# Performance work log

Measured on AMD Instinct MI355X. Metric: run time of the kernel, lower is better.

The kernel has to match this reference:

```python
import jax, jax.numpy as jnp
import numpy as np

B, P, U = 512, 24, 24
IN_T, IN_I, IN_O = 768, 2048, 512
INI = 512            # ini_hidden_dim for all three input linears
H = 1000             # BiLSTM hidden; embed_d = 2*H
E = 2 * H            # embed_d = 2000
INIA = 512           # agg init_linear out dim
HA = 1000            # agg BiLSTM hidden


def _bilstm1(x, W, b):
    """Single-step bidirectional LSTM from zero initial state.
    x: [..., D], W: [2, 4H, D] (fwd/bwd stacked), b: [2, 4H] (b_ih+b_hh).
    With h0=c0=0: gates = x@W_ih^T + b; c = sigmoid(i)*tanh(g); h = sigmoid(o)*tanh(c).
    Returns [..., 2H] (fwd then bwd, matching torch bidirectional concat)."""
    g = jnp.einsum('...d,khd->...kh', x, W) + b          # [..., 2, 4H]
    i, f, gg, o = jnp.split(g, 4, axis=-1)
    c = jax.nn.sigmoid(i) * jnp.tanh(gg)
    h = jax.nn.sigmoid(o) * jnp.tanh(c)                  # [..., 2, H]
    return h.reshape(h.shape[:-2] + (2 * h.shape[-1],))


def _lin(x, W, b):
    return x @ W.T + b


def setup_inputs() -> dict:
    key = jax.random.key(0)
    ks = iter(jax.random.split(key, 48))
    s = 0.05
    def w(*shape):
        return jax.random.normal(next(ks), shape, jnp.float32) * s
    def dat(*shape):
        return jax.random.normal(next(ks), shape, jnp.float32)
    inp = {
        'c_text': dat(B, IN_T), 'c_image': dat(B, IN_I),
        'p_text': dat(B, P, IN_T), 'p_image': dat(B, P, IN_I),
        'u_text': dat(B, U, IN_T), 'u_other': dat(B, U, IN_O),
        # shared per-type input linears
        'W_lt': w(INI, IN_T), 'b_lt': w(INI),
        'W_li': w(INI, IN_I), 'b_li': w(INI),
        'W_lo': w(INI, IN_O), 'b_lo': w(INI),
        # per-type BiLSTMs (fwd/bwd stacked on axis 0)
        'lstm_t_W': w(2, 4 * H, INI), 'lstm_t_b': w(2, 4 * H),
        'lstm_i_W': w(2, 4 * H, INI), 'lstm_i_b': w(2, 4 * H),
        'lstm_o_W': w(2, 4 * H, INI), 'lstm_o_b': w(2, 4 * H),
        # SameType_Agg stacks (user and post)
        'ua_lin_W': w(INIA, E), 'ua_lin_b': w(INIA),
        'ua_lstm_W': w(2, 4 * HA, INIA), 'ua_lstm_b': w(2, 4 * HA),
        'ua_out_W': w(E, 2 * HA), 'ua_out_b': w(E),
        'pa_lin_W': w(INIA, E), 'pa_lin_b': w(INIA),
        'pa_lstm_W': w(2, 4 * HA, INIA), 'pa_lstm_b': w(2, 4 * HA),
        'pa_out_W': w(E, 2 * HA), 'pa_out_b': w(E),
        # attention vector for post-type center nodes
        'p_att': w(2 * E, 1),
    }
    return inp


def reference(c_text, c_image, p_text, p_image, u_text, u_other,
              W_lt, b_lt, W_li, b_li, W_lo, b_lo,
              lstm_t_W, lstm_t_b, lstm_i_W, lstm_i_b, lstm_o_W, lstm_o_b,
              ua_lin_W, ua_lin_b, ua_lstm_W, ua_lstm_b, ua_out_W, ua_out_b,
              pa_lin_W, pa_lin_b, pa_lstm_W, pa_lstm_b, pa_out_W, pa_out_b,
              p_att):
    def post_birnn(text, image):
        # cat along seq dim of two len-1 outputs then mean over seq == average
        ht = _bilstm1(_lin(text, W_lt, b_lt), lstm_t_W, lstm_t_b)
        hi = _bilstm1(_lin(image, W_li, b_li), lstm_i_W, lstm_i_b)
        return 0.5 * (ht + hi)                            # [..., E]

    def user_birnn(text, other):
        ht = _bilstm1(_lin(text, W_lt, b_lt), lstm_t_W, lstm_t_b)
        ho = _bilstm1(_lin(other, W_lo, b_lo), lstm_o_W, lstm_o_b)
        return 0.5 * (ht + ho)

    def same_type_agg(ce, lW, lb, sW, sb, oW, ob):
        h = _bilstm1(_lin(ce, lW, lb), sW, sb)            # [B, N, 2*HA]
        out = _lin(h, oW, ob)                             # [B, N, E]
        return out.mean(axis=1)                           # mean over neighbors

    c = post_birnn(c_text, c_image)                       # [B, E] (center = post)
    u_agg = same_type_agg(user_birnn(u_text, u_other),
                          ua_lin_W, ua_lin_b, ua_lstm_W, ua_lstm_b, ua_out_W, ua_out_b)
    p_agg = same_type_agg(post_birnn(p_text, p_image),
                          pa_lin_W, pa_lin_b, pa_lstm_W, pa_lstm_b, pa_out_W, pa_out_b)

    pairs = jnp.stack([jnp.concatenate([c, c], -1),
                       jnp.concatenate([c, u_agg], -1),
                       jnp.concatenate([c, p_agg], -1)], axis=1)   # [B, 3, 2E]
    att = jax.nn.leaky_relu(pairs @ p_att, 0.01)          # [B, 3, 1]
    wts = jax.nn.softmax(att, axis=1)[..., 0]             # [B, 3]
    emb3 = jnp.stack([c, u_agg, p_agg], axis=1)           # [B, 3, E]
    return jnp.einsum('bk,bke->be', wts, emb3)            # [B, E]
```

## Files before the change

### kernel.cpp

```cpp
#include <hip/hip_runtime.h>
#include <hip/hip_bf16.h>


typedef __hip_bfloat16 bf16;
typedef __attribute__((ext_vector_type(8))) short short8;
typedef __attribute__((ext_vector_type(4))) float f32x4;

__device__ __forceinline__ float bf2f(bf16 x){ return __bfloat162float(x); }
__device__ __forceinline__ bf16  f2bf(float x){ return __float2bfloat16(x); }

__device__ __forceinline__ void gld16(const bf16* g, bf16* l){
  __builtin_amdgcn_global_load_lds(
      (const __attribute__((address_space(1))) void*)g,
      (__attribute__((address_space(3))) void*)l, 16, 0, 0);
}

__device__ __forceinline__ void barrier_raw(){ asm volatile("s_barrier" ::: "memory"); }
__device__ __forceinline__ void wait_vm0(){ asm volatile("s_waitcnt vmcnt(0)" ::: "memory"); }
__device__ __forceinline__ void wait_vm3(){ asm volatile("s_waitcnt vmcnt(3)" ::: "memory"); }
__device__ __forceinline__ void wait_vm4(){ asm volatile("s_waitcnt vmcnt(4)" ::: "memory"); }

__device__ __forceinline__ float sigm(float x){ return 1.0f/(1.0f + __expf(-x)); }
__device__ __forceinline__ float tanhfast(float x){
  x = fminf(fmaxf(x, -15.f), 15.f);
  float e = __expf(2.f*x);
  return (e-1.f)/(e+1.f);
}

struct CvtPtrs { const float* p[25]; };
__constant__ long CVT_CUM[26] = {0, 98304, 98432, 360576, 360704, 426240,
  426368, 1450368, 1452368, 2476368, 2478368, 3502368, 3504368, 3760368,
  3760496, 4784496, 4786496, 5786496, 5786996, 6042996, 6043124, 7067124,
  7069124, 8069124, 8069624, 8070624};

__global__ __launch_bounds__(256) void cvt_all(CvtPtrs P, bf16* __restrict__ arena)
{
  long g = (long)blockIdx.x * 256 + threadIdx.x;
  if (g >= 8070624l) return;
  int lo = 0, hi = 24;
  while (lo < hi) { int mid = (lo + hi + 1) >> 1; if (g >= CVT_CUM[mid]) lo = mid; else hi = mid - 1; }
  long rel = (g - CVT_CUM[lo]) * 4;
  float4 v = *(const float4*)(P.p[lo] + rel);
  union { bf16 h[4]; uint2 u; } t;
  t.h[0]=f2bf(v.x); t.h[1]=f2bf(v.y); t.h[2]=f2bf(v.z); t.h[3]=f2bf(v.w);
  *(uint2*)(arena + CVT_CUM[lo]*4 + rel) = t.u;
}

__global__ __launch_bounds__(256) void gemm_linA32(
    const float* __restrict__ A, const float* __restrict__ A2, int splitx,
    const bf16* __restrict__ Bt, const bf16* __restrict__ bias,
    bf16* __restrict__ C, int M, int N, int K, int lda, int ldb, int ldc)
{
  __shared__ bf16 sm[2][(128+128)*32];
  const int tid  = threadIdx.x;
  const int wave = tid >> 6, lane = tid & 63;
  const int wr = (wave >> 1) * 64, wc = (wave & 1) * 64;
  const int ln = lane & 15, lq = lane >> 4;
  const long m0 = (long)blockIdx.x * 128;
  const int  n0 = blockIdx.y * 128;

  const float* Abase; long mrow;
  if ((int)blockIdx.x < splitx) { Abase = A;  mrow = m0; }
  else { Abase = A2; mrow = (long)((int)blockIdx.x - splitx) * 128; }

  const int arow = tid >> 1, ahalf = (tid & 1) * 16;
  const float* pA = Abase + (mrow + arow) * (long)lda + ahalf;
  const int sAoff = arow * 32 + ahalf;
  const int ch = (tid & 3) * 8;
  int colA = n0 + (tid >> 2);       colA = (colA < N) ? colA : (N - 1);
  int colB = n0 + (tid >> 2) + 64;  colB = (colB < N) ? colB : (N - 1);
  const bf16* pB0 = Bt + (long)colA * ldb + ch;
  const bf16* pB1 = Bt + (long)colB * ldb + ch;
  const int sB0 = 128*32 + tid * 8, sB1 = 128*32 + (tid + 256) * 8;

  auto cvtA = [&](bf16* dst, float4 v0, float4 v1, float4 v2, float4 v3){
    union { bf16 h[16]; short8 q[2]; } u;
    u.h[0]=f2bf(v0.x); u.h[1]=f2bf(v0.y); u.h[2]=f2bf(v0.z); u.h[3]=f2bf(v0.w);
    u.h[4]=f2bf(v1.x); u.h[5]=f2bf(v1.y); u.h[6]=f2bf(v1.z); u.h[7]=f2bf(v1.w);
    u.h[8]=f2bf(v2.x); u.h[9]=f2bf(v2.y); u.h[10]=f2bf(v2.z); u.h[11]=f2bf(v2.w);
    u.h[12]=f2bf(v3.x); u.h[13]=f2bf(v3.y); u.h[14]=f2bf(v3.z); u.h[15]=f2bf(v3.w);
    *(short8*)(dst)     = u.q[0];
    *(short8*)(dst + 8) = u.q[1];
  };

  const int ksteps = K >> 5;
  {
    float4 v0 = *(const float4*)(pA);
    float4 v1 = *(const float4*)(pA + 4);
    float4 v2 = *(const float4*)(pA + 8);
    float4 v3 = *(const float4*)(pA + 12);
    cvtA(sm[0] + sAoff, v0, v1, v2, v3);
    gld16(pB0, sm[0] + sB0);
    gld16(pB1, sm[0] + sB1);
    pA += 32; pB0 += 32; pB1 += 32;
  }
  __syncthreads();

  f32x4 acc[4][4] = {};
  for (int ks = 0; ks < ksteps; ++ks) {
    const bf16* S = sm[ks & 1];
    bf16* Sn = sm[(ks + 1) & 1];
    const bool stage = (ks + 1 < ksteps);
    float4 v0, v1, v2, v3;
    if (stage) {
      v0 = *(const float4*)(pA);
      v1 = *(const float4*)(pA + 4);
      v2 = *(const float4*)(pA + 8);
      v3 = *(const float4*)(pA + 12);
      gld16(pB0, Sn + sB0);
      gld16(pB1, Sn + sB1);
      pA += 32; pB0 += 32; pB1 += 32;
    }
    const bf16* As = S; const bf16* Bs = S + 128*32;
    short8 af[4], bv[4];
#pragma unroll
    for (int i = 0; i < 4; ++i)
      af[i] = *(const short8*)(As + (wr + i*16 + ln) * 32 + lq * 8);
#pragma unroll
    for (int j = 0; j < 4; ++j)
      bv[j] = *(const short8*)(Bs + (wc + j*16 + ln) * 32 + lq * 8);
#pragma unroll
    for (int i = 0; i < 4; ++i)
#pragma unroll
      for (int j = 0; j < 4; ++j)
        acc[i][j] = __builtin_amdgcn_mfma_f32_16x16x32_bf16(af[i], bv[j], acc[i][j], 0, 0, 0);
    if (stage) cvtA(Sn + sAoff, v0, v1, v2, v3);
    __syncthreads();
  }
#pragma unroll
  for (int j = 0; j < 4; ++j) {
    int n = n0 + wc + j * 16 + ln;
    if (n < N) {
      float bvv = bf2f(bias[n]);
#pragma unroll
      for (int i = 0; i < 4; ++i)
#pragma unroll
        for (int r = 0; r < 4; ++r) {
          long m = m0 + wr + i * 16 + lq * 4 + r;
          C[m * ldc + n] = f2bf(acc[i][j][r] + bvv);
        }
    } else if (n < ldc) {
#pragma unroll
      for (int i = 0; i < 4; ++i)
#pragma unroll
        for (int r = 0; r < 4; ++r) {
          long m = m0 + wr + i * 16 + lq * 4 + r;
          C[m * ldc + n] = f2bf(0.f);
        }
    }
  }
}

__global__ __launch_bounds__(256) void gemm_lin(
    const bf16* __restrict__ A, const bf16* __restrict__ Bt,
    const bf16* __restrict__ bias, bf16* __restrict__ C,
    int M, int N, int K, int lda, int ldb, int ldc)
{
  __shared__ bf16 sm[2][(128+128)*32];
  const int tid  = threadIdx.x;
  const int wave = tid >> 6, lane = tid & 63;
  const int wr = (wave >> 1) * 64, wc = (wave & 1) * 64;
  const int ln = lane & 15, lq = lane >> 4;
  const long m0 = (long)blockIdx.x * 128;
  const int  n0 = blockIdx.y * 128;

  const int ch = (tid & 3) * 8;
  const bf16* pA0 = A + (m0 + (tid >> 2)) * (long)lda + ch;
  const bf16* pA1 = A + (m0 + (tid >> 2) + 64) * (long)lda + ch;
  int colA = n0 + (tid >> 2);       colA = (colA < N) ? colA : (N - 1);
  int colB = n0 + (tid >> 2) + 64;  colB = (colB < N) ? colB : (N - 1);
  const bf16* pB0 = Bt + (long)colA * ldb + ch;
  const bf16* pB1 = Bt + (long)colB * ldb + ch;
  const int sA0 = tid * 8, sA1 = (tid + 256) * 8;
  const int sB0 = 128*32 + tid * 8, sB1 = 128*32 + (tid + 256) * 8;

  const int ksteps = (K + 31) >> 5;
  {
    gld16(pA0, sm[0] + sA0); gld16(pA1, sm[0] + sA1);
    gld16(pB0, sm[0] + sB0); gld16(pB1, sm[0] + sB1);
    pA0 += 32; pA1 += 32; pB0 += 32; pB1 += 32;
  }
  __syncthreads();

  f32x4 acc[4][4] = {};
  for (int ks = 0; ks < ksteps; ++ks) {
    const bf16* S = sm[ks & 1];
    bf16* Sn = sm[(ks + 1) & 1];
    if (ks + 1 < ksteps) {
      gld16(pA0, Sn + sA0); gld16(pA1, Sn + sA1);
      gld16(pB0, Sn + sB0); gld16(pB1, Sn + sB1);
      pA0 += 32; pA1 += 32; pB0 += 32; pB1 += 32;
    }
    const bf16* As = S; const bf16* Bs = S + 128*32;
    short8 af[4], bv[4];
#pragma unroll
    for (int i = 0; i < 4; ++i)
      af[i] = *(const short8*)(As + (wr + i*16 + ln) * 32 + lq * 8);
#pragma unroll
    for (int j = 0; j < 4; ++j)
      bv[j] = *(const short8*)(Bs + (wc + j*16 + ln) * 32 + lq * 8);
#pragma unroll
    for (int i = 0; i < 4; ++i)
#pragma unroll
      for (int j = 0; j < 4; ++j)
        acc[i][j] = __builtin_amdgcn_mfma_f32_16x16x32_bf16(af[i], bv[j], acc[i][j], 0, 0, 0);
    __syncthreads();
  }
#pragma unroll
  for (int j = 0; j < 4; ++j) {
    int n = n0 + wc + j * 16 + ln;
    if (n < N) {
      float bvv = bf2f(bias[n]);
#pragma unroll
      for (int i = 0; i < 4; ++i)
#pragma unroll
        for (int r = 0; r < 4; ++r) {
          long m = m0 + wr + i * 16 + lq * 4 + r;
          C[m * ldc + n] = f2bf(acc[i][j][r] + bvv);
        }
    } else if (n < ldc) {
#pragma unroll
      for (int i = 0; i < 4; ++i)
#pragma unroll
        for (int r = 0; r < 4; ++r) {
          long m = m0 + wr + i * 16 + lq * 4 + r;
          C[m * ldc + n] = f2bf(0.f);
        }
    }
  }
}

__global__ __launch_bounds__(256) void gemm_out_f32(
    const bf16* __restrict__ A0, const bf16* __restrict__ A1,
    const bf16* __restrict__ B0, const bf16* __restrict__ B1,
    const bf16* __restrict__ b0, const bf16* __restrict__ b1,
    float* __restrict__ C0, float* __restrict__ C1)
{
  __shared__ bf16 sm[2][(128+128)*32];
  const int tid  = threadIdx.x;
  const int wave = tid >> 6, lane = tid & 63;
  const int wr = (wave >> 1) * 64, wc = (wave & 1) * 64;
  const int ln = lane & 15, lq = lane >> 4;
  const int seg = blockIdx.x >> 2;
  const long m0 = (long)(blockIdx.x & 3) * 128;
  const int  n0 = blockIdx.y * 128;
  const int N = 2000, lda = 2016, ldb = 2000, ldc = 2000;

  const bf16* A    = seg ? A1 : A0;
  const bf16* Bt   = seg ? B1 : B0;
  const bf16* bias = seg ? b1 : b0;
  float*      C    = seg ? C1 : C0;

  const int ch = (tid & 3) * 8;
  const bf16* pA0 = A + (m0 + (tid >> 2)) * (long)lda + ch;
  const bf16* pA1 = A + (m0 + (tid >> 2) + 64) * (long)lda + ch;
  int colA = n0 + (tid >> 2);       colA = (colA < N) ? colA : (N - 1);
  int colB = n0 + (tid >> 2) + 64;  colB = (colB < N) ? colB : (N - 1);
  const bf16* pB0 = Bt + (long)colA * ldb + ch;
  const bf16* pB1 = Bt + (long)colB * ldb + ch;
  const int sA0 = tid * 8, sA1 = (tid + 256) * 8;
  const int sB0 = 128*32 + tid * 8, sB1 = 128*32 + (tid + 256) * 8;

  {
    gld16(pA0, sm[0] + sA0); gld16(pA1, sm[0] + sA1);
    gld16(pB0, sm[0] + sB0); gld16(pB1, sm[0] + sB1);
    pA0 += 32; pA1 += 32; pB0 += 32; pB1 += 32;
  }
  __syncthreads();

  f32x4 acc[4][4] = {};
  for (int ks = 0; ks < 63; ++ks) {
    const bf16* S = sm[ks & 1];
    bf16* Sn = sm[(ks + 1) & 1];
    if (ks + 1 < 63) {
      gld16(pA0, Sn + sA0); gld16(pA1, Sn + sA1);
      gld16(pB0, Sn + sB0); gld16(pB1, Sn + sB1);
      pA0 += 32; pA1 += 32; pB0 += 32; pB1 += 32;
    }
    const bf16* As = S; const bf16* Bs = S + 128*32;
    short8 af[4], bv[4];
#pragma unroll
    for (int i = 0; i < 4; ++i)
      af[i] = *(const short8*)(As + (wr + i*16 + ln) * 32 + lq * 8);
#pragma unroll
    for (int j = 0; j < 4; ++j)
      bv[j] = *(const short8*)(Bs + (wc + j*16 + ln) * 32 + lq * 8);
#pragma unroll
    for (int i = 0; i < 4; ++i)
#pragma unroll
      for (int j = 0; j < 4; ++j)
        acc[i][j] = __builtin_amdgcn_mfma_f32_16x16x32_bf16(af[i], bv[j], acc[i][j], 0, 0, 0);
    __syncthreads();
  }
#pragma unroll
  for (int j = 0; j < 4; ++j) {
    int n = n0 + wc + j * 16 + ln;
    if (n < N) {
      float bvv = bf2f(bias[n]);
#pragma unroll
      for (int i = 0; i < 4; ++i)
#pragma unroll
        for (int r = 0; r < 4; ++r) {
          long m = m0 + wr + i * 16 + lq * 4 + r;
          C[m * ldc + n] = acc[i][j][r] + bvv;
        }
    }
  }
}

__global__ __launch_bounds__(256) void gemm_lstm(
    const bf16* __restrict__ A, const bf16* __restrict__ W,
    const bf16* __restrict__ bvec, const bf16* __restrict__ other,
    bf16* __restrict__ Hout, int ldo, int ldc, int combine)
{
  __shared__ bf16 sm[2][(128+96)*32];
  const int tid  = threadIdx.x;
  const int wave = tid >> 6, lane = tid & 63;
  const int wr = (wave >> 1) * 64, wc = (wave & 1) * 48;
  const int ln = lane & 15, lq = lane >> 4;
  const long m0 = (long)blockIdx.x * 128;
  const int dir = blockIdx.y >> 5, jb = blockIdx.y & 31;

  const int ch = (tid & 3) * 8;
  const bf16* pA0 = A + (m0 + (tid >> 2)) * 512 + ch;
  const bf16* pA1 = A + (m0 + (tid >> 2) + 64) * 512 + ch;
  auto brow = [&](int t) -> long {
    int tc = t >> 2;
    int grp = tc / 48, wi = tc % 48, cf = wi >> 4;
    int jj = jb * 32 + grp * 16 + (wi & 15);
    jj = (jj < 1000) ? jj : 999;
    return (long)(dir * 4000 + cf * 1000 + (cf ? 1000 : 0) + jj);
  };
  const bf16* pB0 = W + brow(tid) * 512 + ch;
  const bf16* pB1 = W + brow(tid + 256) * 512 + ch;
  const int sA0 = tid * 8, sA1 = (tid + 256) * 8;
  const int sB0 = 128*32 + tid * 8, sB1 = 128*32 + (tid + 256) * 8;
  const bool doB1 = (tid < 128);

  {
    gld16(pA0, sm[0] + sA0); gld16(pA1, sm[0] + sA1);
    gld16(pB0, sm[0] + sB0);
    if (doB1) gld16(pB1, sm[0] + sB1);
    pA0 += 32; pA1 += 32; pB0 += 32; pB1 += 32;
  }

  f32x4 acc[4][3] = {};
  for (int ks = 0; ks < 16; ++ks) {
    const bf16* S = sm[ks & 1];
    bf16* Sn = sm[(ks + 1) & 1];
    const bool stage = (ks + 1 < 16);
    if (stage) {
      gld16(pA0, Sn + sA0); gld16(pA1, Sn + sA1);
      gld16(pB0, Sn + sB0);
      if (doB1) gld16(pB1, Sn + sB1);
      pA0 += 32; pA1 += 32; pB0 += 32; pB1 += 32;
    }
    if (!stage)      wait_vm0();
    else if (doB1)   wait_vm4();
    else             wait_vm3();
    barrier_raw();
    const bf16* As = S; const bf16* Bs = S + 128*32;
    short8 af[4], bv[3];
#pragma unroll
    for (int i = 0; i < 4; ++i)
      af[i] = *(const short8*)(As + (wr + i*16 + ln) * 32 + lq * 8);
#pragma unroll
    for (int j = 0; j < 3; ++j)
      bv[j] = *(const short8*)(Bs + (wc + j*16 + ln) * 32 + lq * 8);
#pragma unroll
    for (int i = 0; i < 4; ++i)
#pragma unroll
      for (int j = 0; j < 3; ++j)
        acc[i][j] = __builtin_amdgcn_mfma_f32_16x16x32_bf16(af[i], bv[j], acc[i][j], 0, 0, 0);
    barrier_raw();
  }
  const int jj  = jb * 32 + (wave & 1) * 16 + ln;
  const int jc  = (jj < 1000) ? jj : 999;
  const float bI = bf2f(bvec[dir * 4000 + jc]);
  const float bG = bf2f(bvec[dir * 4000 + 2000 + jc]);
  const float bO = bf2f(bvec[dir * 4000 + 3000 + jc]);
  const int col = dir * 1000 + jj;
  const bool sv = (jj < 1000);
  const bool sz = (!sv) && (dir == 1) && (col < ldc);
  if (!sv && !sz) return;
#pragma unroll
  for (int i = 0; i < 4; ++i)
#pragma unroll
    for (int r = 0; r < 4; ++r) {
      long m = m0 + wr + i * 16 + lq * 4 + r;
      float h = 0.f;
      if (sv) {
        float gi = acc[i][0][r] + bI;
        float gg = acc[i][1][r] + bG;
        float go = acc[i][2][r] + bO;
        float cc = sigm(gi) * tanhfast(gg);
        h = sigm(go) * tanhfast(cc);
        if (combine) h = 0.5f * (h + bf2f(other[m * ldo + col]));
      }
      Hout[m * ldc + col] = f2bf(h);
    }
}

__global__ __launch_bounds__(256) void meanh(const bf16* __restrict__ X, bf16* __restrict__ Y)
{
  long idx = (long)blockIdx.x * 256 + threadIdx.x;
  if (idx >= 512l * 2016) return;
  long b = idx / 2016, e = idx % 2016;
  const bf16* p = X + b * 24 * 2016 + e;
  float s = 0.f;
#pragma unroll
  for (int n = 0; n < 24; ++n) s += bf2f(p[(long)n * 2016]);
  Y[idx] = f2bf(s * (1.f / 24.f));
}

__global__ __launch_bounds__(256) void attn_mix(
    const bf16* __restrict__ Cm, const float* __restrict__ U,
    const float* __restrict__ P, const float* __restrict__ att,
    float* __restrict__ out, int ldcm)
{
  const int b = blockIdx.x, tid = threadIdx.x;
  __shared__ float red[4][4];
  __shared__ float wsh[3];
  float s0 = 0, s1 = 0, s2 = 0, s3 = 0;
  const long baseC = (long)b * ldcm;
  const long base  = (long)b * 2000;
  for (int e = tid; e < 2000; e += 256) {
    float cv = bf2f(Cm[baseC + e]);
    float al = att[e];
    float ah = att[2000 + e];
    s0 += cv * al; s1 += cv * ah;
    s2 += U[base + e] * ah; s3 += P[base + e] * ah;
  }
#pragma unroll
  for (int o = 32; o; o >>= 1) {
    s0 += __shfl_down(s0, o); s1 += __shfl_down(s1, o);
    s2 += __shfl_down(s2, o); s3 += __shfl_down(s3, o);
  }
  if ((tid & 63) == 0) {
    int w = tid >> 6;
    red[w][0] = s0; red[w][1] = s1; red[w][2] = s2; red[w][3] = s3;
  }
  __syncthreads();
  if (tid == 0) {
    float a0 = 0, a1 = 0, a2 = 0, a3 = 0;
    for (int w = 0; w < 4; ++w) { a0 += red[w][0]; a1 += red[w][1]; a2 += red[w][2]; a3 += red[w][3]; }
    float t0 = a0 + a1, t1 = a0 + a2, t2 = a0 + a3;
    t0 = t0 > 0 ? t0 : 0.01f * t0;
    t1 = t1 > 0 ? t1 : 0.01f * t1;
    t2 = t2 > 0 ? t2 : 0.01f * t2;
    float mx = fmaxf(t0, fmaxf(t1, t2));
    float e0 = __expf(t0 - mx), e1 = __expf(t1 - mx), e2 = __expf(t2 - mx);
    float inv = 1.f / (e0 + e1 + e2);
    wsh[0] = e0 * inv; wsh[1] = e1 * inv; wsh[2] = e2 * inv;
  }
  __syncthreads();
  float w0 = wsh[0], w1 = wsh[1], w2 = wsh[2];
  for (int e = tid; e < 2000; e += 256)
    out[base + e] = w0 * bf2f(Cm[baseC + e]) + w1 * U[base + e] + w2 * P[base + e];
}

extern "C" void kernel_launch(void* const* d_in, const int* in_sizes, int n_in,
                              void* d_out, int out_size, void* d_ws, size_t ws_size,
                              hipStream_t stream)
{
  const float* c_text  = (const float*)d_in[0];
  const float* c_image = (const float*)d_in[1];
  const float* p_text  = (const float*)d_in[2];
  const float* p_image = (const float*)d_in[3];
  const float* u_text  = (const float*)d_in[4];
  const float* u_other = (const float*)d_in[5];
  const float* p_att   = (const float*)d_in[30];
  float* out = (float*)d_out;

  char* ws = (char*)d_ws;
  size_t off = 0;
  auto alloc = [&](size_t bytes) -> char* {
    char* p = ws + off; off += (bytes + 255) & ~(size_t)255; return p;
  };
  bf16* ARENA = (bf16*)alloc(32282496ull * 2);
  bf16* BIG1  = (bf16*)alloc(12800ull * 2016 * 2);
  bf16* BIG2  = (bf16*)alloc(12800ull * 2016 * 2);
  bf16* X1    = (bf16*)alloc(12800ull * 512 * 2);
  bf16* X2    = (bf16*)alloc(12800ull * 512 * 2);
  bf16* Yu    = (bf16*)alloc(512ull * 2016 * 2);
  bf16* Yp    = (bf16*)alloc(512ull * 2016 * 2);
  float* UA   = (float*)alloc(512ull * 2000 * 4);
  float* PA   = (float*)alloc(512ull * 2000 * 4);
  (void)ws_size; (void)in_sizes; (void)n_in; (void)out_size;

  const bf16* aW_lt = ARENA + 0;        const bf16* ab_lt = ARENA + 393216;
  const bf16* aW_li = ARENA + 393728;   const bf16* ab_li = ARENA + 1442304;
  const bf16* aW_lo = ARENA + 1442816;  const bf16* ab_lo = ARENA + 1704960;
  const bf16* alt_W = ARENA + 1705472;  const bf16* alt_b = ARENA + 5801472;
  const bf16* ali_W = ARENA + 5809472;  const bf16* ali_b = ARENA + 9905472;
  const bf16* alo_W = ARENA + 9913472;  const bf16* alo_b = ARENA + 14009472;
  const bf16* aua_lin_W  = ARENA + 14017472; const bf16* aua_lin_b  = ARENA + 15041472;
  const bf16* aua_lstm_W = ARENA + 15041984; const bf16* aua_lstm_b = ARENA + 19137984;
  const bf16* aua_out_W  = ARENA + 19145984; const bf16* aua_out_b  = ARENA + 23145984;
  const bf16* apa_lin_W  = ARENA + 23147984; const bf16* apa_lin_b  = ARENA + 24171984;
  const bf16* apa_lstm_W = ARENA + 24172496; const bf16* apa_lstm_b = ARENA + 28268496;
  const bf16* apa_out_W  = ARENA + 28276496; const bf16* apa_out_b  = ARENA + 32276496;

  CvtPtrs cp;
  for (int i = 0; i < 25; ++i) cp.p[i] = (const float*)d_in[6 + i];
  cvt_all<<<dim3(31527), dim3(256), 0, stream>>>(cp, ARENA);

  dim3 blk(256);
  const int NOSPLIT = 1 << 30;

  gemm_linA32<<<dim3(96,4), blk, 0, stream>>>(u_text,  u_text,  NOSPLIT, aW_lt, ab_lt, X1, 12288, 512, 768, 768, 768, 512);
  gemm_linA32<<<dim3(96,4), blk, 0, stream>>>(u_other, u_other, NOSPLIT, aW_lo, ab_lo, X2, 12288, 512, 512, 512, 512, 512);
  gemm_lstm<<<dim3(96,64), blk, 0, stream>>>(X1, alt_W, alt_b, nullptr, BIG1, 2016, 2016, 0);
  gemm_lstm<<<dim3(96,64), blk, 0, stream>>>(X2, alo_W, alo_b, BIG1,    BIG2, 2016, 2016, 1);
  gemm_lin<<<dim3(96,4), blk, 0, stream>>>(BIG2, aua_lin_W, aua_lin_b, X1, 12288, 512, 2000, 2016, 2000, 512);
  gemm_lstm<<<dim3(96,64), blk, 0, stream>>>(X1, aua_lstm_W, aua_lstm_b, nullptr, BIG1, 2016, 2016, 0);
  meanh<<<dim3(4032), blk, 0, stream>>>(BIG1, Yu);

  gemm_linA32<<<dim3(100,4), blk, 0, stream>>>(p_text,  c_text,  96, aW_lt, ab_lt, X1, 12800, 512, 768,  768,  768,  512);
  gemm_linA32<<<dim3(100,4), blk, 0, stream>>>(p_image, c_image, 96, aW_li, ab_li, X2, 12800, 512, 2048, 2048, 2048, 512);
  gemm_lstm<<<dim3(100,64), blk, 0, stream>>>(X1, alt_W, alt_b, nullptr, BIG1, 2016, 2016, 0);
  gemm_lstm<<<dim3(100,64), blk, 0, stream>>>(X2, ali_W, ali_b, BIG1,    BIG2, 2016, 2016, 1);
  gemm_lin<<<dim3(96,4), blk, 0, stream>>>(BIG2, apa_lin_W, apa_lin_b, X1, 12288, 512, 2000, 2016, 2000, 512);
  gemm_lstm<<<dim3(96,64), blk, 0, stream>>>(X1, apa_lstm_W, apa_lstm_b, nullptr, BIG1, 2016, 2016, 0);
  meanh<<<dim3(4032), blk, 0, stream>>>(BIG1, Yp);

  gemm_out_f32<<<dim3(8,16), blk, 0, stream>>>(Yu, Yp, aua_out_W, apa_out_W,
                                               aua_out_b, apa_out_b, UA, PA);
  attn_mix<<<dim3(512), blk, 0, stream>>>(BIG2 + 12288l * 2016, UA, PA, p_att, out, 2016);
}
```

Measured before the change: 1.490 ms.

## Widen LSTM gate GEMM tile to 64 hidden units and swizzle LDS chunks

The fused LSTM gate GEMM now computes 64 hidden units per block (192 weight rows) instead of 32, halving the grid along the hidden dimension and doubling reuse of each staged activation tile. It also XOR-swizzles the 16-byte k-chunks in LDS on both write and read, to reduce bank conflicts on the fragment loads. The cost is more accumulator registers (4x6 tiles), more LDS per block and fewer blocks, which may lower occupancy.

```diff
diff --git a/kernel.cpp b/kernel.cpp
--- a/kernel.cpp
+++ b/kernel.cpp
@@ -17,8 +17,7 @@
 
 __device__ __forceinline__ void barrier_raw(){ asm volatile("s_barrier" ::: "memory"); }
 __device__ __forceinline__ void wait_vm0(){ asm volatile("s_waitcnt vmcnt(0)" ::: "memory"); }
-__device__ __forceinline__ void wait_vm3(){ asm volatile("s_waitcnt vmcnt(3)" ::: "memory"); }
-__device__ __forceinline__ void wait_vm4(){ asm volatile("s_waitcnt vmcnt(4)" ::: "memory"); }
+__device__ __forceinline__ void wait_vm5(){ asm volatile("s_waitcnt vmcnt(5)" ::: "memory"); }
 
 __device__ __forceinline__ float sigm(float x){ return 1.0f/(1.0f + __expf(-x)); }
 __device__ __forceinline__ float tanhfast(float x){
@@ -313,92 +312,96 @@
     const bf16* __restrict__ bvec, const bf16* __restrict__ other,
     bf16* __restrict__ Hout, int ldo, int ldc, int combine)
 {
-  __shared__ bf16 sm[2][(128+96)*32];
+  __shared__ bf16 sm[2][(128+192)*32];
   const int tid  = threadIdx.x;
   const int wave = tid >> 6, lane = tid & 63;
-  const int wr = (wave >> 1) * 64, wc = (wave & 1) * 48;
+  const int wr = (wave >> 1) * 64, wc = (wave & 1) * 96;
   const int ln = lane & 15, lq = lane >> 4;
   const long m0 = (long)blockIdx.x * 128;
-  const int dir = blockIdx.y >> 5, jb = blockIdx.y & 31;
-
-  const int ch = (tid & 3) * 8;
+  const int dir = blockIdx.y >> 4, jb = blockIdx.y & 15;
+
+  const int ch = (((tid & 3) ^ ((tid >> 3) & 3))) * 8;
   const bf16* pA0 = A + (m0 + (tid >> 2)) * 512 + ch;
   const bf16* pA1 = A + (m0 + (tid >> 2) + 64) * 512 + ch;
   auto brow = [&](int t) -> long {
     int tc = t >> 2;
-    int grp = tc / 48, wi = tc % 48, cf = wi >> 4;
-    int jj = jb * 32 + grp * 16 + (wi & 15);
+    int g48 = tc / 48, wi = tc % 48;
+    int cf = wi >> 4;
+    int jj = jb * 64 + g48 * 16 + (wi & 15);
     jj = (jj < 1000) ? jj : 999;
-    return (long)(dir * 4000 + cf * 1000 + (cf ? 1000 : 0) + jj);
+    return (long)(dir * 4000 + (cf ? (cf + 1) * 1000 : 0) + jj);
   };
   const bf16* pB0 = W + brow(tid) * 512 + ch;
   const bf16* pB1 = W + brow(tid + 256) * 512 + ch;
+  const bf16* pB2 = W + brow(tid + 512) * 512 + ch;
   const int sA0 = tid * 8, sA1 = (tid + 256) * 8;
-  const int sB0 = 128*32 + tid * 8, sB1 = 128*32 + (tid + 256) * 8;
-  const bool doB1 = (tid < 128);
+  const int sB0 = 128*32 + tid * 8;
+  const int sB1 = 128*32 + (tid + 256) * 8;
+  const int sB2 = 128*32 + (tid + 512) * 8;
+  const int swz = (lq ^ ((ln >> 1) & 3)) * 8;
 
   {
     gld16(pA0, sm[0] + sA0); gld16(pA1, sm[0] + sA1);
-    gld16(pB0, sm[0] + sB0);
-    if (doB1) gld16(pB1, sm[0] + sB1);
-    pA0 += 32; pA1 += 32; pB0 += 32; pB1 += 32;
-  }
-
-  f32x4 acc[4][3] = {};
+    gld16(pB0, sm[0] + sB0); gld16(pB1, sm[0] + sB1); gld16(pB2, sm[0] + sB2);
+    pA0 += 32; pA1 += 32; pB0 += 32; pB1 += 32; pB2 += 32;
+  }
+
+  f32x4 acc[4][6] = {};
   for (int ks = 0; ks < 16; ++ks) {
     const bf16* S = sm[ks & 1];
     bf16* Sn = sm[(ks + 1) & 1];
     const bool stage = (ks + 1 < 16);
     if (stage) {
       gld16(pA0, Sn + sA0); gld16(pA1, Sn + sA1);
-      gld16(pB0, Sn + sB0);
-      if (doB1) gld16(pB1, Sn + sB1);
-      pA0 += 32; pA1 += 32; pB0 += 32; pB1 += 32;
-    }
-    if (!stage)      wait_vm0();
-    else if (doB1)   wait_vm4();
-    else             wait_vm3();
+      gld16(pB0, Sn + sB0); gld16(pB1, Sn + sB1); gld16(pB2, Sn + sB2);
+      pA0 += 32; pA1 += 32; pB0 += 32; pB1 += 32; pB2 += 32;
+    }
+    if (stage) wait_vm5(); else wait_vm0();
     barrier_raw();
     const bf16* As = S; const bf16* Bs = S + 128*32;
-    short8 af[4], bv[3];
-#pragma unroll
-    for (int i = 0; i < 4; ++i)
-      af[i] = *(const short8*)(As + (wr + i*16 + ln) * 32 + lq * 8);
-#pragma unroll
-    for (int j = 0; j < 3; ++j)
-      bv[j] = *(const short8*)(Bs + (wc + j*16 + ln) * 32 + lq * 8);
-#pragma unroll
-    for (int i = 0; i < 4; ++i)
-#pragma unroll
-      for (int j = 0; j < 3; ++j)
+    short8 af[4], bv[6];
+#pragma unroll
+    for (int i = 0; i < 4; ++i)
+      af[i] = *(const short8*)(As + (wr + i*16 + ln) * 32 + swz);
+#pragma unroll
+    for (int j = 0; j < 6; ++j)
+      bv[j] = *(const short8*)(Bs + (wc + j*16 + ln) * 32 + swz);
+#pragma unroll
+    for (int i = 0; i < 4; ++i)
+#pragma unroll
+      for (int j = 0; j < 6; ++j)
         acc[i][j] = __builtin_amdgcn_mfma_f32_16x16x32_bf16(af[i], bv[j], acc[i][j], 0, 0, 0);
     barrier_raw();
   }
-  const int jj  = jb * 32 + (wave & 1) * 16 + ln;
-  const int jc  = (jj < 1000) ? jj : 999;
-  const float bI = bf2f(bvec[dir * 4000 + jc]);
-  const float bG = bf2f(bvec[dir * 4000 + 2000 + jc]);
-  const float bO = bf2f(bvec[dir * 4000 + 3000 + jc]);
-  const int col = dir * 1000 + jj;
-  const bool sv = (jj < 1000);
-  const bool sz = (!sv) && (dir == 1) && (col < ldc);
-  if (!sv && !sz) return;
-#pragma unroll
-  for (int i = 0; i < 4; ++i)
-#pragma unroll
-    for (int r = 0; r < 4; ++r) {
-      long m = m0 + wr + i * 16 + lq * 4 + r;
-      float h = 0.f;
-      if (sv) {
-        float gi = acc[i][0][r] + bI;
-        float gg = acc[i][1][r] + bG;
-        float go = acc[i][2][r] + bO;
-        float cc = sigm(gi) * tanhfast(gg);
-        h = sigm(go) * tanhfast(cc);
-        if (combine) h = 0.5f * (h + bf2f(other[m * ldo + col]));
+  const int hbase = jb * 64 + (wave & 1) * 32;
+#pragma unroll
+  for (int jg = 0; jg < 2; ++jg) {
+    const int jj = hbase + jg * 16 + ln;
+    const int jc = (jj < 1000) ? jj : 999;
+    const float bI = bf2f(bvec[dir * 4000 + jc]);
+    const float bG = bf2f(bvec[dir * 4000 + 2000 + jc]);
+    const float bO = bf2f(bvec[dir * 4000 + 3000 + jc]);
+    const int col = dir * 1000 + jj;
+    const bool sv = (jj < 1000);
+    const bool sz = (!sv) && (dir == 1) && (col < ldc);
+    if (!sv && !sz) continue;
+#pragma unroll
+    for (int i = 0; i < 4; ++i)
+#pragma unroll
+      for (int r = 0; r < 4; ++r) {
+        long m = m0 + wr + i * 16 + lq * 4 + r;
+        float h = 0.f;
+        if (sv) {
+          float gi = acc[i][jg*3+0][r] + bI;
+          float gg = acc[i][jg*3+1][r] + bG;
+          float go = acc[i][jg*3+2][r] + bO;
+          float cc = sigm(gi) * tanhfast(gg);
+          h = sigm(go) * tanhfast(cc);
+          if (combine) h = 0.5f * (h + bf2f(other[m * ldo + col]));
+        }
+        Hout[m * ldc + col] = f2bf(h);
       }
-      Hout[m * ldc + col] = f2bf(h);
-    }
+  }
 }
 
 __global__ __launch_bounds__(256) void meanh(const bf16* __restrict__ X, bf16* __restrict__ Y)
@@ -510,18 +513,18 @@
 
   gemm_linA32<<<dim3(96,4), blk, 0, stream>>>(u_text,  u_text,  NOSPLIT, aW_lt, ab_lt, X1, 12288, 512, 768, 768, 768, 512);
   gemm_linA32<<<dim3(96,4), blk, 0, stream>>>(u_other, u_other, NOSPLIT, aW_lo, ab_lo, X2, 12288, 512, 512, 512, 512, 512);
-  gemm_lstm<<<dim3(96,64), blk, 0, stream>>>(X1, alt_W, alt_b, nullptr, BIG1, 2016, 2016, 0);
-  gemm_lstm<<<dim3(96,64), blk, 0, stream>>>(X2, alo_W, alo_b, BIG1,    BIG2, 2016, 2016, 1);
+  gemm_lstm<<<dim3(96,32), blk, 0, stream>>>(X1, alt_W, alt_b, nullptr, BIG1, 2016, 2016, 0);
+  gemm_lstm<<<dim3(96,32), blk, 0, stream>>>(X2, alo_W, alo_b, BIG1,    BIG2, 2016, 2016, 1);
   gemm_lin<<<dim3(96,4), blk, 0, stream>>>(BIG2, aua_lin_W, aua_lin_b, X1, 12288, 512, 2000, 2016, 2000, 512);
-  gemm_lstm<<<dim3(96,64), blk, 0, stream>>>(X1, aua_lstm_W, aua_lstm_b, nullptr, BIG1, 2016, 2016, 0);
+  gemm_lstm<<<dim3(96,32), blk, 0, stream>>>(X1, aua_lstm_W, aua_lstm_b, nullptr, BIG1, 2016, 2016, 0);
   meanh<<<dim3(4032), blk, 0, stream>>>(BIG1, Yu);
 
   gemm_linA32<<<dim3(100,4), blk, 0, stream>>>(p_text,  c_text,  96, aW_lt, ab_lt, X1, 12800, 512, 768,  768,  768,  512);
   gemm_linA32<<<dim3(100,4), blk, 0, stream>>>(p_image, c_image, 96, aW_li, ab_li, X2, 12800, 512, 2048, 2048, 2048, 512);
-  gemm_lstm<<<dim3(100,64), blk, 0, stream>>>(X1, alt_W, alt_b, nullptr, BIG1, 2016, 2016, 0);
-  gemm_lstm<<<dim3(100,64), blk, 0, stream>>>(X2, ali_W, ali_b, BIG1,    BIG2, 2016, 2016, 1);
+  gemm_lstm<<<dim3(100,32), blk, 0, stream>>>(X1, alt_W, alt_b, nullptr, BIG1, 2016, 2016, 0);
+  gemm_lstm<<<dim3(100,32), blk, 0, stream>>>(X2, ali_W, ali_b, BIG1,    BIG2, 2016, 2016, 1);
   gemm_lin<<<dim3(96,4), blk, 0, stream>>>(BIG2, apa_lin_W, apa_lin_b, X1, 12288, 512, 2000, 2016, 2000, 512);
-  gemm_lstm<<<dim3(96,64), blk, 0, stream>>>(X1, apa_lstm_W, apa_lstm_b, nullptr, BIG1, 2016, 2016, 0);
+  gemm_lstm<<<dim3(96,32), blk, 0, stream>>>(X1, apa_lstm_W, apa_lstm_b, nullptr, BIG1, 2016, 2016, 0);
   meanh<<<dim3(4032), blk, 0, stream>>>(BIG1, Yp);
 
   gemm_out_f32<<<dim3(8,16), blk, 0, stream>>>(Yu, Yp, aua_out_W, apa_out_W,
```

New measurement: 1.530 ms. 1.03x slower.
